# Kernel tuning notes

Measured on AMD Instinct MI355X. Metric: run time of the kernel, lower is better.

## Reference

```python
import jax, jax.numpy as jnp
import numpy as np

HEADS = 16
HIDDEN = 1024
D_K = HIDDEN // HEADS


def setup_inputs() -> dict:
    key = jax.random.key(0)
    ks = jax.random.split(key, 13)
    B, S, H = 2, 2048, HIDDEN
    scale = 1.0 / np.sqrt(H)
    inp = {
        "q": jax.random.normal(ks[0], (B, S, H), jnp.float32),
        "k": jax.random.normal(ks[1], (B, S, H), jnp.float32),
        "v": jax.random.normal(ks[2], (B, S, H), jnp.float32),
        "mask": jax.random.randint(ks[3], (B, S, S), 0, 2, jnp.int32),
        # torch Linear weights: [out, in], y = x @ W.T + b
        "Wq": jax.random.normal(ks[4], (H, H), jnp.float32) * scale,
        "bq": jax.random.normal(ks[5], (H,), jnp.float32) * 0.01,
        "Wk": jax.random.normal(ks[6], (H, H), jnp.float32) * scale,
        "bk": jax.random.normal(ks[7], (H,), jnp.float32) * 0.01,
        "Wv": jax.random.normal(ks[8], (H, H), jnp.float32) * scale,
        "bv": jax.random.normal(ks[9], (H,), jnp.float32) * 0.01,
        "Wo": jax.random.normal(ks[10], (H, H), jnp.float32) * scale,
        "bo": jax.random.normal(ks[11], (H,), jnp.float32) * 0.01,
    }
    return inp


def _split_heads(x, B):
    # (B, S, H) -> (B, heads, S, d_k)
    return x.reshape(B, -1, HEADS, D_K).transpose(0, 2, 1, 3)


def reference(q, k, v, mask, Wq, bq, Wk, bk, Wv, bv, Wo, bo):
    B, S, H = q.shape
    qh = _split_heads(q @ Wq.T + bq, B)
    kh = _split_heads(k @ Wk.T + bk, B)
    vh = _split_heads(v @ Wv.T + bv, B)
    inv_sqrt_dk = 1.0 / jnp.sqrt(jnp.asarray(D_K, qh.dtype))
    logits = jnp.einsum("bhqd,bhkd->bhqk", qh, kh) * inv_sqrt_dk
    # faithful to source: masked positions get logit 1e-9 (not -inf)
    m = mask[:, None, :, :]  # broadcast over heads
    logits = jnp.where(m == 0, jnp.asarray(1e-9, logits.dtype), logits)
    scores = jax.nn.softmax(logits, axis=-1)
    o = jnp.einsum("bhqk,bhkd->bhqd", scores, vh)  # (B, heads, S, d_k)
    o = o.transpose(0, 2, 1, 3).reshape(B, S, H)
    return o @ Wo.T + bo
```

## Files before the change

### kernel.cpp

```cpp
#include <hip/hip_runtime.h>

#define SEQ   2048
#define NHEAD 16
#define DKK   64
#define HID   1024

typedef __attribute__((ext_vector_type(8))) short bf16x8;
typedef __attribute__((ext_vector_type(4))) float f32x4;

__device__ __forceinline__ unsigned short f32_bf16(float f) {
    unsigned int u = __builtin_bit_cast(unsigned int, f);
    u += 0x7fffu + ((u >> 16) & 1u);
    return (unsigned short)(u >> 16);
}

__device__ __forceinline__ unsigned int cvt_pk_bf16(float lo, float hi) {
    unsigned int r;
    asm("v_cvt_pk_bf16_f32 %0, %1, %2" : "=v"(r) : "v"(lo), "v"(hi));
    return r;
}

__device__ __forceinline__ float fast_exp2(float x) {
    float r;
    asm("v_exp_f32 %0, %1" : "=v"(r) : "v"(x));
    return r;
}

__device__ __forceinline__ void glds16(const void* g, void* l) {
    __builtin_amdgcn_global_load_lds(
        (const __attribute__((address_space(1))) unsigned int*)g,
        (__attribute__((address_space(3))) unsigned int*)l, 16, 0, 0);
}

__global__ __launch_bounds__(256)
void prep_kernel(const float* __restrict__ q, const float* __restrict__ k,
                 const float* __restrict__ v,
                 const float* __restrict__ Wq, const float* __restrict__ Wk,
                 const float* __restrict__ Wv, const float* __restrict__ Wo,
                 const int* __restrict__ mask,
                 unsigned short* __restrict__ ws, unsigned long long* __restrict__ Mb)
{
    const int bid = blockIdx.x;
    if (bid < 16384) {
        int i = bid * 256 + threadIdx.x;
        const float* src; int off;
        if (i < 1048576)      { src = q;  off = i; }
        else if (i < 2097152) { src = k;  off = i - 1048576; }
        else if (i < 3145728) { src = v;  off = i - 2097152; }
        else if (i < 3407872) { src = Wq; off = i - 3145728; }
        else if (i < 3670016) { src = Wk; off = i - 3407872; }
        else if (i < 3932160) { src = Wv; off = i - 3670016; }
        else                  { src = Wo; off = i - 3932160; }
        float4 a = ((const float4*)src)[off];
        ((uint2*)ws)[i] = make_uint2(cvt_pk_bf16(a.x, a.y), cvt_pk_bf16(a.z, a.w));
    } else {
        int idx = (bid - 16384) * 256 + threadIdx.x;
        const int* src = mask + (size_t)idx * 64;
        unsigned long long wv = 0;
        #pragma unroll
        for (int i = 0; i < 16; ++i) {
            int4 m4 = *(const int4*)(src + i * 4);
            wv |= (unsigned long long)(m4.x != 0) << (i * 4 + 0);
            wv |= (unsigned long long)(m4.y != 0) << (i * 4 + 1);
            wv |= (unsigned long long)(m4.z != 0) << (i * 4 + 2);
            wv |= (unsigned long long)(m4.w != 0) << (i * 4 + 3);
        }
        Mb[idx] = wv;
    }
}

__global__ __launch_bounds__(256, 2)
void proj_kernel(const unsigned short* __restrict__ xq, const unsigned short* __restrict__ xk,
                 const unsigned short* __restrict__ xv,
                 const unsigned short* __restrict__ Wqb, const unsigned short* __restrict__ Wkb,
                 const unsigned short* __restrict__ Wvb,
                 const float* __restrict__ bq_, const float* __restrict__ bk_,
                 const float* __restrict__ bv_,
                 unsigned short* __restrict__ Qh, unsigned short* __restrict__ Kh,
                 unsigned short* __restrict__ Vh)
{
    const int z = blockIdx.z;
    const unsigned short* X; const unsigned short* W; const float* bias;
    if (z == 0)      { X = xq; W = Wqb; bias = bq_; }
    else if (z == 1) { X = xk; W = Wkb; bias = bk_; }
    else             { X = xv; W = Wvb; bias = bv_; }

    const int m0 = blockIdx.x * 128;
    const int n0 = blockIdx.y * 128;
    const int tid  = threadIdx.x;
    const int lane = tid & 63, wid = tid >> 6;
    const int wm = (wid >> 1) * 64, wn = (wid & 1) * 64;
    const int l15 = lane & 15, quad = lane >> 4;

    __shared__ __align__(16) unsigned short As[2][128 * 32];
    __shared__ __align__(16) unsigned short Bs[2][128 * 32];

    const int r0 = tid >> 2, cg = tid & 3;
    const unsigned short* gA = X + (size_t)(m0 + r0) * HID + ((cg ^ (r0 & 3)) * 8);
    const unsigned short* gB = W + (size_t)(n0 + r0) * HID + ((cg ^ (r0 & 3)) * 8);

    const int cgsel = (quad ^ (l15 & 3)) * 8;

    f32x4 acc[4][4];
    #pragma unroll
    for (int i = 0; i < 4; ++i)
        #pragma unroll
        for (int j = 0; j < 4; ++j)
            acc[i][j] = f32x4{0.f, 0.f, 0.f, 0.f};

    glds16(gA, &As[0][tid * 8]);
    glds16(gA + (size_t)64 * HID, &As[0][(tid + 256) * 8]);
    glds16(gB, &Bs[0][tid * 8]);
    glds16(gB + (size_t)64 * HID, &Bs[0][(tid + 256) * 8]);
    __syncthreads();

    for (int k0 = 0; k0 < HID; k0 += 32) {
        const int cur = (k0 >> 5) & 1;
        if (k0 + 32 < HID) {
            const int nb = cur ^ 1;
            glds16(gA + k0 + 32, &As[nb][tid * 8]);
            glds16(gA + (size_t)64 * HID + k0 + 32, &As[nb][(tid + 256) * 8]);
            glds16(gB + k0 + 32, &Bs[nb][tid * 8]);
            glds16(gB + (size_t)64 * HID + k0 + 32, &Bs[nb][(tid + 256) * 8]);
        }

        bf16x8 af[4], bfr[4];
        #pragma unroll
        for (int mi = 0; mi < 4; ++mi)
            af[mi] = *(const bf16x8*)&As[cur][(wm + mi * 16 + l15) * 32 + cgsel];
        #pragma unroll
        for (int ni = 0; ni < 4; ++ni)
            bfr[ni] = *(const bf16x8*)&Bs[cur][(wn + ni * 16 + l15) * 32 + cgsel];
        __builtin_amdgcn_s_setprio(1);
        #pragma unroll
        for (int mi = 0; mi < 4; ++mi)
            #pragma unroll
            for (int ni = 0; ni < 4; ++ni)
                acc[mi][ni] = __builtin_amdgcn_mfma_f32_16x16x32_bf16(
                    af[mi], bfr[ni], acc[mi][ni], 0, 0, 0);
        __builtin_amdgcn_s_setprio(0);
        __syncthreads();
    }

    const float QSCALE = 0.18033688f;
    #pragma unroll
    for (int mi = 0; mi < 4; ++mi) {
        #pragma unroll
        for (int ni = 0; ni < 4; ++ni) {
            int n = n0 + wn + ni * 16 + l15;
            float bv = bias[n];
            int hh = n >> 6, d = n & 63;
            #pragma unroll
            for (int r = 0; r < 4; ++r) {
                int m = m0 + wm + mi * 16 + quad * 4 + r;
                int bb = m >> 11, s = m & 2047;
                float val = acc[mi][ni][r] + bv;
                if (z == 0)
                    Qh[((size_t)(bb * NHEAD + hh) * SEQ + s) * DKK + d] = f32_bf16(val * QSCALE);
                else if (z == 1)
                    Kh[((size_t)(bb * NHEAD + hh) * SEQ + s) * DKK + d] = f32_bf16(val);
                else
                    Vh[((size_t)(bb * NHEAD + hh) * SEQ + s) * DKK + d] = f32_bf16(val);
            }
        }
    }
}

__global__ __launch_bounds__(256)
void vtrans_kernel(const unsigned short* __restrict__ Vh, unsigned short* __restrict__ Vt)
{
    __shared__ unsigned int T[64 * 32];
    const int bh = blockIdx.y;
    const int s0 = blockIdx.x * 64;
    const int tid = threadIdx.x;
    const unsigned short* src = Vh + ((size_t)bh * SEQ + s0) * DKK;
    unsigned short* dst = Vt + (size_t)bh * DKK * SEQ + s0;

    #pragma unroll
    for (int j = 0; j < 2; ++j) {
        int i = tid + j * 256;
        int s = i >> 3, ch = i & 7;
        uint4 d4 = *(const uint4*)(src + (size_t)s * DKK + ch * 8);
        *(uint4*)&T[s * 32 + 4 * (ch ^ (s >> 3))] = d4;
    }
    __syncthreads();
    #pragma unroll
    for (int j = 0; j < 2; ++j) {
        int i = tid + j * 256;
        int d = i >> 3, sb = (i & 7) * 8;
        int d2 = d >> 1, hi = d & 1;
        int g = d2 >> 2, w4 = d2 & 3;
        unsigned int r[8];
        #pragma unroll
        for (int kk = 0; kk < 8; ++kk) {
            int s = sb + kk;
            r[kk] = T[s * 32 + 4 * (g ^ (s >> 3)) + w4];
        }
        uint4 ov;
        if (hi) {
            ov.x = (r[0] >> 16) | (r[1] & 0xffff0000u);
            ov.y = (r[2] >> 16) | (r[3] & 0xffff0000u);
            ov.z = (r[4] >> 16) | (r[5] & 0xffff0000u);
            ov.w = (r[6] >> 16) | (r[7] & 0xffff0000u);
        } else {
            ov.x = (r[0] & 0xffffu) | (r[1] << 16);
            ov.y = (r[2] & 0xffffu) | (r[3] << 16);
            ov.z = (r[4] & 0xffffu) | (r[5] << 16);
            ov.w = (r[6] & 0xffffu) | (r[7] << 16);
        }
        *(uint4*)(dst + (size_t)d * SEQ + sb) = ov;
    }
}

__global__ __launch_bounds__(256, 4)
void attn_kernel(const unsigned short* __restrict__ Qh, const unsigned short* __restrict__ Kh,
                 const unsigned short* __restrict__ Vt,
                 const unsigned long long* __restrict__ Mb,
                 unsigned short* __restrict__ Om)
{
    const int qt = blockIdx.x;
    const int h  = blockIdx.y;
    const int b  = blockIdx.z;
    const int tid  = threadIdx.x;
    const int lane = tid & 63, w = tid >> 6;
    const int l15 = lane & 15, quad = lane >> 4;
    const int q0 = qt * 64;

    const size_t hoff = (size_t)(b * NHEAD + h) * SEQ * DKK;
    const unsigned short* Qp = Qh + hoff;
    const unsigned short* Kp = Kh + hoff;
    const unsigned short* Vp = Vt + hoff;

    __shared__ __align__(16) unsigned short Ks[2][64 * 64];
    __shared__ __align__(16) unsigned short Vs[2][64 * 64];
    __shared__ __align__(16) unsigned short Ps[4][16 * 64];

    const int sr0 = tid >> 3, ss0 = tid & 7;
    const int sr1 = sr0 + 32;
    const unsigned short* Kg0 = Kp + sr0 * DKK + ((ss0 ^ (sr0 & 7)) * 8);
    const unsigned short* Kg1 = Kp + sr1 * DKK + ((ss0 ^ (sr1 & 7)) * 8);
    const unsigned short* Vg0 = Vp + (size_t)sr0 * SEQ + ((ss0 ^ (sr0 & 7)) * 8);
    const unsigned short* Vg1 = Vp + (size_t)sr1 * SEQ + ((ss0 ^ (sr1 & 7)) * 8);

    const int swz0 = ((0 * 4 + quad) ^ (l15 & 7)) * 8;
    const int swz1 = ((1 * 4 + quad) ^ (l15 & 7)) * 8;

    const int xsw = l15 & 14;
    int wadr[4];
    #pragma unroll
    for (int ni = 0; ni < 4; ++ni)
        wadr[ni] = l15 * 64 + (((ni * 4 + quad) ^ xsw) * 4);
    const int padr0 = l15 * 64 + (((quad * 2) ^ xsw) * 4);
    const int padr1 = l15 * 64 + (((8 + quad * 2) ^ xsw) * 4);

    glds16(Kg0, &Ks[0][tid * 8]);
    glds16(Kg1, &Ks[0][2048 + tid * 8]);
    glds16(Vg0, &Vs[0][tid * 8]);
    glds16(Vg1, &Vs[0][2048 + tid * 8]);

    bf16x8 qf[2];
    #pragma unroll
    for (int kc = 0; kc < 2; ++kc)
        qf[kc] = *(const bf16x8*)(Qp + (size_t)(q0 + w * 16 + l15) * DKK + kc * 32 + quad * 8);

    bf16x8 onesf;
    #pragma unroll
    for (int i = 0; i < 8; ++i) onesf[i] = (short)0x3F80;

    f32x4 o_acc[4];
    f32x4 l_acc = f32x4{0.f, 0.f, 0.f, 0.f};
    #pragma unroll
    for (int nd = 0; nd < 4; ++nd) o_acc[nd] = f32x4{0.f, 0.f, 0.f, 0.f};

    const unsigned long long* Mrow =
        Mb + ((size_t)b * SEQ + q0 + w * 16 + l15) * (SEQ / 64);

    __syncthreads();

    for (int kt = 0; kt < SEQ / 64; ++kt) {
        const int cur = kt & 1;
        if (kt < SEQ / 64 - 1) {
            const int nb = cur ^ 1;
            glds16(Kg0 + (kt + 1) * 64 * DKK, &Ks[nb][tid * 8]);
            glds16(Kg1 + (kt + 1) * 64 * DKK, &Ks[nb][2048 + tid * 8]);
            glds16(Vg0 + (kt + 1) * 64,       &Vs[nb][tid * 8]);
            glds16(Vg1 + (kt + 1) * 64,       &Vs[nb][2048 + tid * 8]);
        }

        const unsigned long long mwq = Mrow[kt] >> (quad * 4);

        f32x4 st[4];
        #pragma unroll
        for (int ni = 0; ni < 4; ++ni) st[ni] = f32x4{0.f, 0.f, 0.f, 0.f};
        {
            bf16x8 kb[4];
            #pragma unroll
            for (int ni = 0; ni < 4; ++ni)
                kb[ni] = *(const bf16x8*)&Ks[cur][(ni * 16 + l15) * 64 + swz0];
            __builtin_amdgcn_s_setprio(1);
            #pragma unroll
            for (int ni = 0; ni < 4; ++ni)
                st[ni] = __builtin_amdgcn_mfma_f32_16x16x32_bf16(kb[ni], qf[0], st[ni], 0, 0, 0);
            __builtin_amdgcn_s_setprio(0);
            #pragma unroll
            for (int ni = 0; ni < 4; ++ni)
                kb[ni] = *(const bf16x8*)&Ks[cur][(ni * 16 + l15) * 64 + swz1];
            __builtin_amdgcn_s_setprio(1);
            #pragma unroll
            for (int ni = 0; ni < 4; ++ni)
                st[ni] = __builtin_amdgcn_mfma_f32_16x16x32_bf16(kb[ni], qf[1], st[ni], 0, 0, 0);
            __builtin_amdgcn_s_setprio(0);
        }

        #pragma unroll
        for (int ni = 0; ni < 4; ++ni) {
            const unsigned int b4 = (unsigned int)(mwq >> (ni * 16)) & 0xFu;
            float p0 = (b4 & 1u) ? fast_exp2(st[ni][0]) : 1.0f;
            float p1 = (b4 & 2u) ? fast_exp2(st[ni][1]) : 1.0f;
            float p2 = (b4 & 4u) ? fast_exp2(st[ni][2]) : 1.0f;
            float p3 = (b4 & 8u) ? fast_exp2(st[ni][3]) : 1.0f;
            *(uint2*)&Ps[w][wadr[ni]] = make_uint2(cvt_pk_bf16(p0, p1), cvt_pk_bf16(p2, p3));
        }

        {
            bf16x8 pa = *(const bf16x8*)&Ps[w][padr0];
            bf16x8 vb[4];
            #pragma unroll
            for (int nd = 0; nd < 4; ++nd)
                vb[nd] = *(const bf16x8*)&Vs[cur][(nd * 16 + l15) * 64 + swz0];
            __builtin_amdgcn_s_setprio(1);
            l_acc = __builtin_amdgcn_mfma_f32_16x16x32_bf16(pa, onesf, l_acc, 0, 0, 0);
            #pragma unroll
            for (int nd = 0; nd < 4; ++nd)
                o_acc[nd] = __builtin_amdgcn_mfma_f32_16x16x32_bf16(pa, vb[nd], o_acc[nd], 0, 0, 0);
            __builtin_amdgcn_s_setprio(0);

            pa = *(const bf16x8*)&Ps[w][padr1];
            #pragma unroll
            for (int nd = 0; nd < 4; ++nd)
                vb[nd] = *(const bf16x8*)&Vs[cur][(nd * 16 + l15) * 64 + swz1];
            __builtin_amdgcn_s_setprio(1);
            l_acc = __builtin_amdgcn_mfma_f32_16x16x32_bf16(pa, onesf, l_acc, 0, 0, 0);
            #pragma unroll
            for (int nd = 0; nd < 4; ++nd)
                o_acc[nd] = __builtin_amdgcn_mfma_f32_16x16x32_bf16(pa, vb[nd], o_acc[nd], 0, 0, 0);
            __builtin_amdgcn_s_setprio(0);
        }

        __syncthreads();
    }

    #pragma unroll
    for (int r = 0; r < 4; ++r) {
        float rinv = 1.0f / l_acc[r];
        int row = q0 + w * 16 + quad * 4 + r;
        #pragma unroll
        for (int nd = 0; nd < 4; ++nd)
            Om[((size_t)b * SEQ + row) * HID + h * DKK + nd * 16 + l15] =
                f32_bf16(o_acc[nd][r] * rinv);
    }
}

__global__ __launch_bounds__(256, 2)
void outproj_kernel(const unsigned short* __restrict__ Om, const unsigned short* __restrict__ Wob,
                    const float* __restrict__ bo_, float* __restrict__ out)
{
    const int m0 = blockIdx.x * 128;
    const int n0 = blockIdx.y * 64;
    const int tid  = threadIdx.x;
    const int lane = tid & 63, wid = tid >> 6;
    const int wm = (wid >> 1) * 64, wn = (wid & 1) * 32;
    const int l15 = lane & 15, quad = lane >> 4;

    __shared__ __align__(16) unsigned short As[2][128 * 32];
    __shared__ __align__(16) unsigned short Bs[2][64 * 32];

    const int r0 = tid >> 2, cg = tid & 3;
    const unsigned short* gA = Om + (size_t)(m0 + r0) * HID + ((cg ^ (r0 & 3)) * 8);
    const unsigned short* gB = Wob + (size_t)(n0 + r0) * HID + ((cg ^ (r0 & 3)) * 8);
    const int cgsel = (quad ^ (l15 & 3)) * 8;

    f32x4 acc[4][2];
    #pragma unroll
    for (int i = 0; i < 4; ++i)
        #pragma unroll
        for (int j = 0; j < 2; ++j)
            acc[i][j] = f32x4{0.f, 0.f, 0.f, 0.f};

    glds16(gA, &As[0][tid * 8]);
    glds16(gA + (size_t)64 * HID, &As[0][(tid + 256) * 8]);
    glds16(gB, &Bs[0][tid * 8]);
    __syncthreads();

    for (int k0 = 0; k0 < HID; k0 += 32) {
        const int cur = (k0 >> 5) & 1;
        if (k0 + 32 < HID) {
            const int nb = cur ^ 1;
            glds16(gA + k0 + 32, &As[nb][tid * 8]);
            glds16(gA + (size_t)64 * HID + k0 + 32, &As[nb][(tid + 256) * 8]);
            glds16(gB + k0 + 32, &Bs[nb][tid * 8]);
        }

        bf16x8 af[4], bfr[2];
        #pragma unroll
        for (int mi = 0; mi < 4; ++mi)
            af[mi] = *(const bf16x8*)&As[cur][(wm + mi * 16 + l15) * 32 + cgsel];
        #pragma unroll
        for (int ni = 0; ni < 2; ++ni)
            bfr[ni] = *(const bf16x8*)&Bs[cur][(wn + ni * 16 + l15) * 32 + cgsel];
        __builtin_amdgcn_s_setprio(1);
        #pragma unroll
        for (int mi = 0; mi < 4; ++mi)
            #pragma unroll
            for (int ni = 0; ni < 2; ++ni)
                acc[mi][ni] = __builtin_amdgcn_mfma_f32_16x16x32_bf16(
                    af[mi], bfr[ni], acc[mi][ni], 0, 0, 0);
        __builtin_amdgcn_s_setprio(0);
        __syncthreads();
    }

    #pragma unroll
    for (int mi = 0; mi < 4; ++mi) {
        #pragma unroll
        for (int ni = 0; ni < 2; ++ni) {
            int n = n0 + wn + ni * 16 + l15;
            float bv = bo_[n];
            #pragma unroll
            for (int r = 0; r < 4; ++r) {
                int m = m0 + wm + mi * 16 + quad * 4 + r;
                out[(size_t)m * HID + n] = acc[mi][ni][r] + bv;
            }
        }
    }
}

extern "C" void kernel_launch(void* const* d_in, const int* in_sizes, int n_in,
                              void* d_out, int out_size, void* d_ws, size_t ws_size,
                              hipStream_t stream) {
    const float* q    = (const float*)d_in[0];
    const float* k    = (const float*)d_in[1];
    const float* v    = (const float*)d_in[2];
    const int*   mask = (const int*)  d_in[3];
    const float* Wq   = (const float*)d_in[4];
    const float* bq   = (const float*)d_in[5];
    const float* Wk   = (const float*)d_in[6];
    const float* bk   = (const float*)d_in[7];
    const float* Wv   = (const float*)d_in[8];
    const float* bv   = (const float*)d_in[9];
    const float* Wo   = (const float*)d_in[10];
    const float* bo   = (const float*)d_in[11];
    float* out = (float*)d_out;

    unsigned short* ws  = (unsigned short*)d_ws;
    unsigned short* qb  = ws;
    unsigned short* kbx = ws + 4194304;
    unsigned short* vbx = ws + 8388608;
    unsigned short* Wqb = ws + 12582912;
    unsigned short* Wkb = ws + 13631488;
    unsigned short* Wvb = ws + 14680064;
    unsigned short* Wob = ws + 15728640;
    unsigned short* Qh  = ws + 16777216;
    unsigned short* Kh  = ws + 20971520;
    unsigned short* Vt  = ws + 25165824;
    unsigned short* Om  = ws;
    unsigned long long* Mb = (unsigned long long*)(ws + 29360128);
    unsigned short* Vh  = (unsigned short*)d_out;

    prep_kernel<<<dim3(16896), 256, 0, stream>>>(q, k, v, Wq, Wk, Wv, Wo, mask, ws, Mb);

    proj_kernel<<<dim3(32, 8, 3), 256, 0, stream>>>(qb, kbx, vbx, Wqb, Wkb, Wvb,
                                                    bq, bk, bv, Qh, Kh, Vh);
    vtrans_kernel<<<dim3(32, 32), 256, 0, stream>>>(Vh, Vt);
    attn_kernel<<<dim3(32, NHEAD, 2), 256, 0, stream>>>(Qh, Kh, Vt, Mb, Om);
    outproj_kernel<<<dim3(32, 16), 256, 0, stream>>>(Om, Wob, bo, out);
}
```

Before: 279.3 us.

## Triple-buffer GEMM loads with vmcnt waits, ballot mask packing, prefetch mask words

The projection and output-projection GEMMs move from double to triple buffering in shared memory. Loads are issued two stages ahead, and a partial s_waitcnt vmcnt plus a raw s_barrier replaces the full __syncthreads, so more global-to-LDS traffic overlaps with MFMA work. Mask bit-packing now uses coalesced per-lane loads and a wavefront ballot instead of each thread reading 64 contiguous ints. The attention kernel also prefetches the next mask word one iteration early. This adds LDS usage per block, which may lower occupancy, and the partial waitcnt logic depends on global_load_lds ordering being correct.

```diff
diff --git a/kernel.cpp b/kernel.cpp
--- a/kernel.cpp
+++ b/kernel.cpp
@@ -31,6 +31,11 @@
         (const __attribute__((address_space(1))) unsigned int*)g,
         (__attribute__((address_space(3))) unsigned int*)l, 16, 0, 0);
 }
+
+#define WAITCNT_VM(N)                                          \
+    asm volatile("s_waitcnt vmcnt(" #N ")" ::: "memory");      \
+    __builtin_amdgcn_sched_barrier(0);                         \
+    __builtin_amdgcn_s_barrier();
 
 __global__ __launch_bounds__(256)
 void prep_kernel(const float* __restrict__ q, const float* __restrict__ k,
@@ -54,18 +59,16 @@
         float4 a = ((const float4*)src)[off];
         ((uint2*)ws)[i] = make_uint2(cvt_pk_bf16(a.x, a.y), cvt_pk_bf16(a.z, a.w));
     } else {
-        int idx = (bid - 16384) * 256 + threadIdx.x;
-        const int* src = mask + (size_t)idx * 64;
-        unsigned long long wv = 0;
-        #pragma unroll
-        for (int i = 0; i < 16; ++i) {
-            int4 m4 = *(const int4*)(src + i * 4);
-            wv |= (unsigned long long)(m4.x != 0) << (i * 4 + 0);
-            wv |= (unsigned long long)(m4.y != 0) << (i * 4 + 1);
-            wv |= (unsigned long long)(m4.z != 0) << (i * 4 + 2);
-            wv |= (unsigned long long)(m4.w != 0) << (i * 4 + 3);
-        }
-        Mb[idx] = wv;
+        const int g    = (bid - 16384) * 4 + (threadIdx.x >> 6);
+        const int lane = threadIdx.x & 63;
+        const int* src = mask + (size_t)g * 4096;
+        unsigned long long* dstw = Mb + (size_t)g * 64;
+        #pragma unroll 4
+        for (int j = 0; j < 64; ++j) {
+            int m = src[j * 64 + lane];
+            unsigned long long wv = __ballot(m != 0);
+            if (lane == 0) dstw[j] = wv;
+        }
     }
 }
 
@@ -92,8 +95,8 @@
     const int wm = (wid >> 1) * 64, wn = (wid & 1) * 64;
     const int l15 = lane & 15, quad = lane >> 4;
 
-    __shared__ __align__(16) unsigned short As[2][128 * 32];
-    __shared__ __align__(16) unsigned short Bs[2][128 * 32];
+    __shared__ __align__(16) unsigned short As[3][128 * 32];
+    __shared__ __align__(16) unsigned short Bs[3][128 * 32];
 
     const int r0 = tid >> 2, cg = tid & 3;
     const unsigned short* gA = X + (size_t)(m0 + r0) * HID + ((cg ^ (r0 & 3)) * 8);
@@ -108,29 +111,21 @@
         for (int j = 0; j < 4; ++j)
             acc[i][j] = f32x4{0.f, 0.f, 0.f, 0.f};
 
-    glds16(gA, &As[0][tid * 8]);
-    glds16(gA + (size_t)64 * HID, &As[0][(tid + 256) * 8]);
-    glds16(gB, &Bs[0][tid * 8]);
-    glds16(gB + (size_t)64 * HID, &Bs[0][(tid + 256) * 8]);
-    __syncthreads();
-
-    for (int k0 = 0; k0 < HID; k0 += 32) {
-        const int cur = (k0 >> 5) & 1;
-        if (k0 + 32 < HID) {
-            const int nb = cur ^ 1;
-            glds16(gA + k0 + 32, &As[nb][tid * 8]);
-            glds16(gA + (size_t)64 * HID + k0 + 32, &As[nb][(tid + 256) * 8]);
-            glds16(gB + k0 + 32, &Bs[nb][tid * 8]);
-            glds16(gB + (size_t)64 * HID + k0 + 32, &Bs[nb][(tid + 256) * 8]);
-        }
-
+    auto STAGE = [&](int ks, int buf) {
+        const int off = ks * 32;
+        glds16(gA + off,                      &As[buf][tid * 8]);
+        glds16(gA + (size_t)64 * HID + off,   &As[buf][(tid + 256) * 8]);
+        glds16(gB + off,                      &Bs[buf][tid * 8]);
+        glds16(gB + (size_t)64 * HID + off,   &Bs[buf][(tid + 256) * 8]);
+    };
+    auto COMPUTE = [&](int buf) {
         bf16x8 af[4], bfr[4];
         #pragma unroll
         for (int mi = 0; mi < 4; ++mi)
-            af[mi] = *(const bf16x8*)&As[cur][(wm + mi * 16 + l15) * 32 + cgsel];
+            af[mi] = *(const bf16x8*)&As[buf][(wm + mi * 16 + l15) * 32 + cgsel];
         #pragma unroll
         for (int ni = 0; ni < 4; ++ni)
-            bfr[ni] = *(const bf16x8*)&Bs[cur][(wn + ni * 16 + l15) * 32 + cgsel];
+            bfr[ni] = *(const bf16x8*)&Bs[buf][(wn + ni * 16 + l15) * 32 + cgsel];
         __builtin_amdgcn_s_setprio(1);
         #pragma unroll
         for (int mi = 0; mi < 4; ++mi)
@@ -139,8 +134,19 @@
                 acc[mi][ni] = __builtin_amdgcn_mfma_f32_16x16x32_bf16(
                     af[mi], bfr[ni], acc[mi][ni], 0, 0, 0);
         __builtin_amdgcn_s_setprio(0);
-        __syncthreads();
-    }
+    };
+
+    STAGE(0, 0); STAGE(1, 1);
+    WAITCNT_VM(4)
+
+    for (int i = 0; i < 30; ++i) {
+        STAGE(i + 2, (i + 2) % 3);
+        COMPUTE(i % 3);
+        WAITCNT_VM(4)
+    }
+    COMPUTE(0);
+    WAITCNT_VM(0)
+    COMPUTE(1);
 
     const float QSCALE = 0.18033688f;
     #pragma unroll
@@ -274,20 +280,23 @@
 
     const unsigned long long* Mrow =
         Mb + ((size_t)b * SEQ + q0 + w * 16 + l15) * (SEQ / 64);
+    unsigned long long mw_cur = Mrow[0];
 
     __syncthreads();
 
     for (int kt = 0; kt < SEQ / 64; ++kt) {
         const int cur = kt & 1;
+        unsigned long long mw_nxt = 0ull;
         if (kt < SEQ / 64 - 1) {
             const int nb = cur ^ 1;
             glds16(Kg0 + (kt + 1) * 64 * DKK, &Ks[nb][tid * 8]);
             glds16(Kg1 + (kt + 1) * 64 * DKK, &Ks[nb][2048 + tid * 8]);
             glds16(Vg0 + (kt + 1) * 64,       &Vs[nb][tid * 8]);
             glds16(Vg1 + (kt + 1) * 64,       &Vs[nb][2048 + tid * 8]);
-        }
-
-        const unsigned long long mwq = Mrow[kt] >> (quad * 4);
+            mw_nxt = Mrow[kt + 1];
+        }
+
+        const unsigned long long mwq = mw_cur >> (quad * 4);
 
         f32x4 st[4];
         #pragma unroll
@@ -347,6 +356,7 @@
             __builtin_amdgcn_s_setprio(0);
         }
 
+        mw_cur = mw_nxt;
         __syncthreads();
     }
 
@@ -372,8 +382,8 @@
     const int wm = (wid >> 1) * 64, wn = (wid & 1) * 32;
     const int l15 = lane & 15, quad = lane >> 4;
 
-    __shared__ __align__(16) unsigned short As[2][128 * 32];
-    __shared__ __align__(16) unsigned short Bs[2][64 * 32];
+    __shared__ __align__(16) unsigned short As[3][128 * 32];
+    __shared__ __align__(16) unsigned short Bs[3][64 * 32];
 
     const int r0 = tid >> 2, cg = tid & 3;
     const unsigned short* gA = Om + (size_t)(m0 + r0) * HID + ((cg ^ (r0 & 3)) * 8);
@@ -387,27 +397,20 @@
         for (int j = 0; j < 2; ++j)
             acc[i][j] = f32x4{0.f, 0.f, 0.f, 0.f};
 
-    glds16(gA, &As[0][tid * 8]);
-    glds16(gA + (size_t)64 * HID, &As[0][(tid + 256) * 8]);
-    glds16(gB, &Bs[0][tid * 8]);
-    __syncthreads();
-
-    for (int k0 = 0; k0 < HID; k0 += 32) {
-        const int cur = (k0 >> 5) & 1;
-        if (k0 + 32 < HID) {
-            const int nb = cur ^ 1;
-            glds16(gA + k0 + 32, &As[nb][tid * 8]);
-            glds16(gA + (size_t)64 * HID + k0 + 32, &As[nb][(tid + 256) * 8]);
-            glds16(gB + k0 + 32, &Bs[nb][tid * 8]);
-        }
-
+    auto STAGE = [&](int ks, int buf) {
+        const int off = ks * 32;
+        glds16(gA + off,                    &As[buf][tid * 8]);
+        glds16(gA + (size_t)64 * HID + off, &As[buf][(tid + 256) * 8]);
+        glds16(gB + off,                    &Bs[buf][tid * 8]);
+    };
+    auto COMPUTE = [&](int buf) {
         bf16x8 af[4], bfr[2];
         #pragma unroll
         for (int mi = 0; mi < 4; ++mi)
-            af[mi] = *(const bf16x8*)&As[cur][(wm + mi * 16 + l15) * 32 + cgsel];
+            af[mi] = *(const bf16x8*)&As[buf][(wm + mi * 16 + l15) * 32 + cgsel];
         #pragma unroll
         for (int ni = 0; ni < 2; ++ni)
-            bfr[ni] = *(const bf16x8*)&Bs[cur][(wn + ni * 16 + l15) * 32 + cgsel];
+            bfr[ni] = *(const bf16x8*)&Bs[buf][(wn + ni * 16 + l15) * 32 + cgsel];
         __builtin_amdgcn_s_setprio(1);
         #pragma unroll
         for (int mi = 0; mi < 4; ++mi)
@@ -416,8 +419,19 @@
                 acc[mi][ni] = __builtin_amdgcn_mfma_f32_16x16x32_bf16(
                     af[mi], bfr[ni], acc[mi][ni], 0, 0, 0);
         __builtin_amdgcn_s_setprio(0);
-        __syncthreads();
-    }
+    };
+
+    STAGE(0, 0); STAGE(1, 1);
+    WAITCNT_VM(3)
+
+    for (int i = 0; i < 30; ++i) {
+        STAGE(i + 2, (i + 2) % 3);
+        COMPUTE(i % 3);
+        WAITCNT_VM(3)
+    }
+    COMPUTE(0);
+    WAITCNT_VM(0)
+    COMPUTE(1);
 
     #pragma unroll
     for (int mi = 0; mi < 4; ++mi) {
```

After: 292.3 us. +4.6%, slower.

## Double query rows per attention block and pack mask bits with wave ballot

Applied to the files above, without the earlier changes.

Each attention wave now handles 32 query rows (two 16-row groups) instead of 16. This halves the grid and reuses each K/V LDS tile across twice as many MFMAs, cutting K/V global loads and LDS fills per query. The mask words for the next tile are prefetched one iteration ahead. The mask-packing prep stage now uses coalesced per-wave loads with __ballot instead of strided int4 reads per thread. The costs are higher register pressure (launch bound lowered to 2 blocks per CU) and only 512 attention blocks, which may underfill the GPU.

```diff
diff --git a/kernel.cpp b/kernel.cpp
--- a/kernel.cpp
+++ b/kernel.cpp
@@ -54,18 +54,16 @@
         float4 a = ((const float4*)src)[off];
         ((uint2*)ws)[i] = make_uint2(cvt_pk_bf16(a.x, a.y), cvt_pk_bf16(a.z, a.w));
     } else {
-        int idx = (bid - 16384) * 256 + threadIdx.x;
-        const int* src = mask + (size_t)idx * 64;
-        unsigned long long wv = 0;
-        #pragma unroll
-        for (int i = 0; i < 16; ++i) {
-            int4 m4 = *(const int4*)(src + i * 4);
-            wv |= (unsigned long long)(m4.x != 0) << (i * 4 + 0);
-            wv |= (unsigned long long)(m4.y != 0) << (i * 4 + 1);
-            wv |= (unsigned long long)(m4.z != 0) << (i * 4 + 2);
-            wv |= (unsigned long long)(m4.w != 0) << (i * 4 + 3);
-        }
-        Mb[idx] = wv;
+        const int g    = (bid - 16384) * 4 + (threadIdx.x >> 6);
+        const int lane = threadIdx.x & 63;
+        const int* src = mask + (size_t)g * 4096;
+        unsigned long long* dstw = Mb + (size_t)g * 64;
+        #pragma unroll 4
+        for (int j = 0; j < 64; ++j) {
+            int m = src[j * 64 + lane];
+            unsigned long long wv = __ballot(m != 0);
+            if (lane == 0) dstw[j] = wv;
+        }
     }
 }
 
@@ -212,7 +210,7 @@
     }
 }
 
-__global__ __launch_bounds__(256, 4)
+__global__ __launch_bounds__(256, 2)
 void attn_kernel(const unsigned short* __restrict__ Qh, const unsigned short* __restrict__ Kh,
                  const unsigned short* __restrict__ Vt,
                  const unsigned long long* __restrict__ Mb,
@@ -224,7 +222,7 @@
     const int tid  = threadIdx.x;
     const int lane = tid & 63, w = tid >> 6;
     const int l15 = lane & 15, quad = lane >> 4;
-    const int q0 = qt * 64;
+    const int q0 = qt * 128;
 
     const size_t hoff = (size_t)(b * NHEAD + h) * SEQ * DKK;
     const unsigned short* Qp = Qh + hoff;
@@ -233,7 +231,7 @@
 
     __shared__ __align__(16) unsigned short Ks[2][64 * 64];
     __shared__ __align__(16) unsigned short Vs[2][64 * 64];
-    __shared__ __align__(16) unsigned short Ps[4][16 * 64];
+    __shared__ __align__(16) unsigned short Ps[4][2][16 * 64];
 
     const int sr0 = tid >> 3, ss0 = tid & 7;
     const int sr1 = sr0 + 32;
@@ -258,40 +256,50 @@
     glds16(Vg0, &Vs[0][tid * 8]);
     glds16(Vg1, &Vs[0][2048 + tid * 8]);
 
-    bf16x8 qf[2];
-    #pragma unroll
-    for (int kc = 0; kc < 2; ++kc)
-        qf[kc] = *(const bf16x8*)(Qp + (size_t)(q0 + w * 16 + l15) * DKK + kc * 32 + quad * 8);
+    bf16x8 qf[2][2];
+    #pragma unroll
+    for (int g = 0; g < 2; ++g)
+        #pragma unroll
+        for (int kc = 0; kc < 2; ++kc)
+            qf[g][kc] = *(const bf16x8*)(Qp + (size_t)(q0 + w * 32 + g * 16 + l15) * DKK
+                                         + kc * 32 + quad * 8);
 
     bf16x8 onesf;
     #pragma unroll
     for (int i = 0; i < 8; ++i) onesf[i] = (short)0x3F80;
 
-    f32x4 o_acc[4];
-    f32x4 l_acc = f32x4{0.f, 0.f, 0.f, 0.f};
-    #pragma unroll
-    for (int nd = 0; nd < 4; ++nd) o_acc[nd] = f32x4{0.f, 0.f, 0.f, 0.f};
-
-    const unsigned long long* Mrow =
-        Mb + ((size_t)b * SEQ + q0 + w * 16 + l15) * (SEQ / 64);
+    f32x4 o_acc[2][4];
+    f32x4 l_acc[2];
+    #pragma unroll
+    for (int g = 0; g < 2; ++g) {
+        l_acc[g] = f32x4{0.f, 0.f, 0.f, 0.f};
+        #pragma unroll
+        for (int nd = 0; nd < 4; ++nd) o_acc[g][nd] = f32x4{0.f, 0.f, 0.f, 0.f};
+    }
+
+    const unsigned long long* Mrow0 =
+        Mb + ((size_t)b * SEQ + q0 + w * 32 + l15) * (SEQ / 64);
+    const unsigned long long* Mrow1 = Mrow0 + (size_t)16 * (SEQ / 64);
+    unsigned long long mw0 = Mrow0[0], mw1 = Mrow1[0];
 
     __syncthreads();
 
     for (int kt = 0; kt < SEQ / 64; ++kt) {
         const int cur = kt & 1;
+        unsigned long long mw0n = 0ull, mw1n = 0ull;
         if (kt < SEQ / 64 - 1) {
             const int nb = cur ^ 1;
             glds16(Kg0 + (kt + 1) * 64 * DKK, &Ks[nb][tid * 8]);
             glds16(Kg1 + (kt + 1) * 64 * DKK, &Ks[nb][2048 + tid * 8]);
             glds16(Vg0 + (kt + 1) * 64,       &Vs[nb][tid * 8]);
             glds16(Vg1 + (kt + 1) * 64,       &Vs[nb][2048 + tid * 8]);
-        }
-
-        const unsigned long long mwq = Mrow[kt] >> (quad * 4);
-
-        f32x4 st[4];
-        #pragma unroll
-        for (int ni = 0; ni < 4; ++ni) st[ni] = f32x4{0.f, 0.f, 0.f, 0.f};
+            mw0n = Mrow0[kt + 1];
+            mw1n = Mrow1[kt + 1];
+        }
+
+        f32x4 st0[4], st1[4];
+        #pragma unroll
+        for (int ni = 0; ni < 4; ++ni) { st0[ni] = f32x4{0.f,0.f,0.f,0.f}; st1[ni] = f32x4{0.f,0.f,0.f,0.f}; }
         {
             bf16x8 kb[4];
             #pragma unroll
@@ -299,65 +307,91 @@
                 kb[ni] = *(const bf16x8*)&Ks[cur][(ni * 16 + l15) * 64 + swz0];
             __builtin_amdgcn_s_setprio(1);
             #pragma unroll
-            for (int ni = 0; ni < 4; ++ni)
-                st[ni] = __builtin_amdgcn_mfma_f32_16x16x32_bf16(kb[ni], qf[0], st[ni], 0, 0, 0);
+            for (int ni = 0; ni < 4; ++ni) {
+                st0[ni] = __builtin_amdgcn_mfma_f32_16x16x32_bf16(kb[ni], qf[0][0], st0[ni], 0, 0, 0);
+                st1[ni] = __builtin_amdgcn_mfma_f32_16x16x32_bf16(kb[ni], qf[1][0], st1[ni], 0, 0, 0);
+            }
             __builtin_amdgcn_s_setprio(0);
             #pragma unroll
             for (int ni = 0; ni < 4; ++ni)
                 kb[ni] = *(const bf16x8*)&Ks[cur][(ni * 16 + l15) * 64 + swz1];
             __builtin_amdgcn_s_setprio(1);
             #pragma unroll
-            for (int ni = 0; ni < 4; ++ni)
-                st[ni] = __builtin_amdgcn_mfma_f32_16x16x32_bf16(kb[ni], qf[1], st[ni], 0, 0, 0);
+            for (int ni = 0; ni < 4; ++ni) {
+                st0[ni] = __builtin_amdgcn_mfma_f32_16x16x32_bf16(kb[ni], qf[0][1], st0[ni], 0, 0, 0);
+                st1[ni] = __builtin_amdgcn_mfma_f32_16x16x32_bf16(kb[ni], qf[1][1], st1[ni], 0, 0, 0);
+            }
             __builtin_amdgcn_s_setprio(0);
         }
 
-        #pragma unroll
-        for (int ni = 0; ni < 4; ++ni) {
-            const unsigned int b4 = (unsigned int)(mwq >> (ni * 16)) & 0xFu;
-            float p0 = (b4 & 1u) ? fast_exp2(st[ni][0]) : 1.0f;
-            float p1 = (b4 & 2u) ? fast_exp2(st[ni][1]) : 1.0f;
-            float p2 = (b4 & 4u) ? fast_exp2(st[ni][2]) : 1.0f;
-            float p3 = (b4 & 8u) ? fast_exp2(st[ni][3]) : 1.0f;
-            *(uint2*)&Ps[w][wadr[ni]] = make_uint2(cvt_pk_bf16(p0, p1), cvt_pk_bf16(p2, p3));
-        }
-
         {
-            bf16x8 pa = *(const bf16x8*)&Ps[w][padr0];
+            const unsigned long long mq0 = mw0 >> (quad * 4);
+            const unsigned long long mq1 = mw1 >> (quad * 4);
+            #pragma unroll
+            for (int ni = 0; ni < 4; ++ni) {
+                unsigned int b4 = (unsigned int)(mq0 >> (ni * 16)) & 0xFu;
+                float p0 = (b4 & 1u) ? fast_exp2(st0[ni][0]) : 1.0f;
+                float p1 = (b4 & 2u) ? fast_exp2(st0[ni][1]) : 1.0f;
+                float p2 = (b4 & 4u) ? fast_exp2(st0[ni][2]) : 1.0f;
+                float p3 = (b4 & 8u) ? fast_exp2(st0[ni][3]) : 1.0f;
+                *(uint2*)&Ps[w][0][wadr[ni]] = make_uint2(cvt_pk_bf16(p0, p1), cvt_pk_bf16(p2, p3));
+                b4 = (unsigned int)(mq1 >> (ni * 16)) & 0xFu;
+                p0 = (b4 & 1u) ? fast_exp2(st1[ni][0]) : 1.0f;
+                p1 = (b4 & 2u) ? fast_exp2(st1[ni][1]) : 1.0f;
+                p2 = (b4 & 4u) ? fast_exp2(st1[ni][2]) : 1.0f;
+                p3 = (b4 & 8u) ? fast_exp2(st1[ni][3]) : 1.0f;
+                *(uint2*)&Ps[w][1][wadr[ni]] = make_uint2(cvt_pk_bf16(p0, p1), cvt_pk_bf16(p2, p3));
+            }
+        }
+
+        {
             bf16x8 vb[4];
             #pragma unroll
             for (int nd = 0; nd < 4; ++nd)
                 vb[nd] = *(const bf16x8*)&Vs[cur][(nd * 16 + l15) * 64 + swz0];
+            bf16x8 pa0 = *(const bf16x8*)&Ps[w][0][padr0];
+            bf16x8 pa1 = *(const bf16x8*)&Ps[w][1][padr0];
             __builtin_amdgcn_s_setprio(1);
-            l_acc = __builtin_amdgcn_mfma_f32_16x16x32_bf16(pa, onesf, l_acc, 0, 0, 0);
-            #pragma unroll
-            for (int nd = 0; nd < 4; ++nd)
-                o_acc[nd] = __builtin_amdgcn_mfma_f32_16x16x32_bf16(pa, vb[nd], o_acc[nd], 0, 0, 0);
+            l_acc[0] = __builtin_amdgcn_mfma_f32_16x16x32_bf16(pa0, onesf, l_acc[0], 0, 0, 0);
+            l_acc[1] = __builtin_amdgcn_mfma_f32_16x16x32_bf16(pa1, onesf, l_acc[1], 0, 0, 0);
+            #pragma unroll
+            for (int nd = 0; nd < 4; ++nd) {
+                o_acc[0][nd] = __builtin_amdgcn_mfma_f32_16x16x32_bf16(pa0, vb[nd], o_acc[0][nd], 0, 0, 0);
+                o_acc[1][nd] = __builtin_amdgcn_mfma_f32_16x16x32_bf16(pa1, vb[nd], o_acc[1][nd], 0, 0, 0);
+            }
             __builtin_amdgcn_s_setprio(0);
 
-            pa = *(const bf16x8*)&Ps[w][padr1];
             #pragma unroll
             for (int nd = 0; nd < 4; ++nd)
                 vb[nd] = *(const bf16x8*)&Vs[cur][(nd * 16 + l15) * 64 + swz1];
+            pa0 = *(const bf16x8*)&Ps[w][0][padr1];
+            pa1 = *(const bf16x8*)&Ps[w][1][padr1];
             __builtin_amdgcn_s_setprio(1);
-            l_acc = __builtin_amdgcn_mfma_f32_16x16x32_bf16(pa, onesf, l_acc, 0, 0, 0);
+            l_acc[0] = __builtin_amdgcn_mfma_f32_16x16x32_bf16(pa0, onesf, l_acc[0], 0, 0, 0);
+            l_acc[1] = __builtin_amdgcn_mfma_f32_16x16x32_bf16(pa1, onesf, l_acc[1], 0, 0, 0);
+            #pragma unroll
+            for (int nd = 0; nd < 4; ++nd) {
+                o_acc[0][nd] = __builtin_amdgcn_mfma_f32_16x16x32_bf16(pa0, vb[nd], o_acc[0][nd], 0, 0, 0);
+                o_acc[1][nd] = __builtin_amdgcn_mfma_f32_16x16x32_bf16(pa1, vb[nd], o_acc[1][nd], 0, 0, 0);
+            }
+            __builtin_amdgcn_s_setprio(0);
+        }
+
+        mw0 = mw0n; mw1 = mw1n;
+        __syncthreads();
+    }
+
+    #pragma unroll
+    for (int g = 0; g < 2; ++g) {
+        #pragma unroll
+        for (int r = 0; r < 4; ++r) {
+            float rinv = 1.0f / l_acc[g][r];
+            int row = q0 + w * 32 + g * 16 + quad * 4 + r;
             #pragma unroll
             for (int nd = 0; nd < 4; ++nd)
-                o_acc[nd] = __builtin_amdgcn_mfma_f32_16x16x32_bf16(pa, vb[nd], o_acc[nd], 0, 0, 0);
-            __builtin_amdgcn_s_setprio(0);
-        }
-
-        __syncthreads();
-    }
-
-    #pragma unroll
-    for (int r = 0; r < 4; ++r) {
-        float rinv = 1.0f / l_acc[r];
-        int row = q0 + w * 16 + quad * 4 + r;
-        #pragma unroll
-        for (int nd = 0; nd < 4; ++nd)
-            Om[((size_t)b * SEQ + row) * HID + h * DKK + nd * 16 + l15] =
-                f32_bf16(o_acc[nd][r] * rinv);
+                Om[((size_t)b * SEQ + row) * HID + h * DKK + nd * 16 + l15] =
+                    f32_bf16(o_acc[g][nd][r] * rinv);
+        }
     }
 }
 
@@ -471,6 +505,6 @@
     proj_kernel<<<dim3(32, 8, 3), 256, 0, stream>>>(qb, kbx, vbx, Wqb, Wkb, Wvb,
                                                     bq, bk, bv, Qh, Kh, Vh);
     vtrans_kernel<<<dim3(32, 32), 256, 0, stream>>>(Vh, Vt);
-    attn_kernel<<<dim3(32, NHEAD, 2), 256, 0, stream>>>(Qh, Kh, Vt, Mb, Om);
+    attn_kernel<<<dim3(16, NHEAD, 2), 256, 0, stream>>>(Qh, Kh, Vt, Mb, Om);
     outproj_kernel<<<dim3(32, 16), 256, 0, stream>>>(Om, Wob, bo, out);
 }
```

Measured after the change: 301.5 us. 7.9% more time.

## Pack mask with wave ballots and prefetch mask words with fine-grained waitcnt

Applied to the files above, without the earlier changes.

The mask bit-packing kernel now has each wave read 64 contiguous ints per row and use a ballot to build each 64-bit word, instead of each thread reading 64 strided ints. This makes the mask reads coalesced. In the attention loop, the mask word for the next tile is prefetched alongside the K/V async loads. The full __syncthreads is replaced by an explicit vmcnt wait plus raw s_barrier, so only the older loads are waited on and the next tile's loads stay in flight. The risk is that the hand-counted vmcnt(5) has to match the number of outstanding loads exactly, otherwise the code can race.

```diff
diff --git a/kernel.cpp b/kernel.cpp
--- a/kernel.cpp
+++ b/kernel.cpp
@@ -54,18 +54,16 @@
         float4 a = ((const float4*)src)[off];
         ((uint2*)ws)[i] = make_uint2(cvt_pk_bf16(a.x, a.y), cvt_pk_bf16(a.z, a.w));
     } else {
-        int idx = (bid - 16384) * 256 + threadIdx.x;
-        const int* src = mask + (size_t)idx * 64;
-        unsigned long long wv = 0;
-        #pragma unroll
-        for (int i = 0; i < 16; ++i) {
-            int4 m4 = *(const int4*)(src + i * 4);
-            wv |= (unsigned long long)(m4.x != 0) << (i * 4 + 0);
-            wv |= (unsigned long long)(m4.y != 0) << (i * 4 + 1);
-            wv |= (unsigned long long)(m4.z != 0) << (i * 4 + 2);
-            wv |= (unsigned long long)(m4.w != 0) << (i * 4 + 3);
-        }
-        Mb[idx] = wv;
+        const int g    = (bid - 16384) * 4 + (threadIdx.x >> 6);
+        const int lane = threadIdx.x & 63;
+        const int* src = mask + (size_t)g * 4096;
+        unsigned long long* dstw = Mb + (size_t)g * 64;
+        #pragma unroll 4
+        for (int j = 0; j < 64; ++j) {
+            int m = src[j * 64 + lane];
+            unsigned long long wv = __ballot(m != 0);
+            if (lane == 0) dstw[j] = wv;
+        }
     }
 }
 
@@ -274,20 +272,27 @@
 
     const unsigned long long* Mrow =
         Mb + ((size_t)b * SEQ + q0 + w * 16 + l15) * (SEQ / 64);
-
-    __syncthreads();
+    unsigned long long mw_cur = Mrow[0];
 
     for (int kt = 0; kt < SEQ / 64; ++kt) {
         const int cur = kt & 1;
+        unsigned long long mw_nxt = 0ull;
+
         if (kt < SEQ / 64 - 1) {
             const int nb = cur ^ 1;
             glds16(Kg0 + (kt + 1) * 64 * DKK, &Ks[nb][tid * 8]);
             glds16(Kg1 + (kt + 1) * 64 * DKK, &Ks[nb][2048 + tid * 8]);
             glds16(Vg0 + (kt + 1) * 64,       &Vs[nb][tid * 8]);
             glds16(Vg1 + (kt + 1) * 64,       &Vs[nb][2048 + tid * 8]);
-        }
-
-        const unsigned long long mwq = Mrow[kt] >> (quad * 4);
+            mw_nxt = Mrow[kt + 1];
+            asm volatile("s_waitcnt vmcnt(5)" ::: "memory");
+        } else {
+            asm volatile("s_waitcnt vmcnt(0)" ::: "memory");
+        }
+        __builtin_amdgcn_s_barrier();
+        __builtin_amdgcn_sched_barrier(0);
+
+        const unsigned long long mwq = mw_cur >> (quad * 4);
 
         f32x4 st[4];
         #pragma unroll
@@ -347,7 +352,10 @@
             __builtin_amdgcn_s_setprio(0);
         }
 
-        __syncthreads();
+        mw_cur = mw_nxt;
+
+        __builtin_amdgcn_s_barrier();
+        __builtin_amdgcn_sched_barrier(0);
     }
 
     #pragma unroll
```

Result: slower. 290.7 us (+4.1%).
